# Optimization experiments

Measured on AMD Instinct MI355X. Metric: run time of the kernel, lower is better.

Reference implementation:

```python
import jax, jax.numpy as jnp
import numpy as np

N_Q = 4  # QuantumSampler is hard-wired to 4 qubits (16-dim statevector)


def _build_tables():
    """Static permutation for the CNOT chain and Z-sign table, computed once in numpy."""
    n = N_Q
    dim = 1 << n
    cnots = [(i, (i + 1) % n) for i in range(n)]  # (0,1),(1,2),(2,3),(3,0)
    fmap = np.empty(dim, dtype=np.int64)
    for i in range(dim):
        bits = [(i >> (n - 1 - w)) & 1 for w in range(n)]  # wire w <-> bit (n-1-w)
        for c, t in cnots:
            if bits[c]:
                bits[t] ^= 1
        fmap[i] = sum(b << (n - 1 - w) for w, b in enumerate(bits))
    finv = np.argsort(fmap)  # new_state[j] = old_state[finv[j]]
    signs = np.array([[1.0 - 2.0 * ((j >> (n - 1 - w)) & 1) for w in range(n)]
                      for j in range(dim)], dtype=np.float32)  # <Z_w> signs per basis state
    return jnp.asarray(finv), jnp.asarray(signs)

PERM, SIGNS = _build_tables()


def quantum_gate_probs(q, theta):
    """Simulate: RX(q_w) then RX(theta_w) per wire (angles add), CNOT chain, <Z> per wire, softmax.
    q: [B,4] encoder angles; theta: [4] trainable angles. Returns [B,4] gate probabilities."""
    half = 0.5 * (q + theta)                      # RX(a)RX(b) = RX(a+b)
    c = jnp.cos(half).astype(jnp.complex64)       # amplitude on |0>
    s = (jnp.sin(half).astype(jnp.complex64)) * (-1j)  # amplitude on |1> is -i sin(a/2)
    a = jnp.stack([c, s], axis=-1)                # [B,4,2] single-qubit states
    a0, a1, a2, a3 = a[:, 0], a[:, 1], a[:, 2], a[:, 3]
    # product state |psi> = a0 (x) a1 (x) a2 (x) a3  -> [B,2,2,2,2] -> [B,16]
    st = (a0[:, :, None, None, None] * a1[:, None, :, None, None]
          * a2[:, None, None, :, None] * a3[:, None, None, None, :])
    st = st.reshape(q.shape[0], 16)[:, PERM]      # apply CNOT chain (amplitude permutation)
    probs = st.real ** 2 + st.imag ** 2           # [B,16]
    exps = probs @ SIGNS                          # [B,4] Pauli-Z expectations per wire
    return jax.nn.softmax(exps, axis=-1)


def setup_inputs() -> dict:
    key = jax.random.key(0)
    ks = jax.random.split(key, 8)
    T, B, D, H = 256, 128, 1024, 1024
    inputs = jax.random.normal(ks[0], (T, B, D), dtype=jnp.float32)
    sc_d = 1.0 / np.sqrt(D)
    sc_h = 1.0 / np.sqrt(H)
    return {
        "inputs": inputs,
        "Wi": jax.random.normal(ks[1], (H, D), dtype=jnp.float32) * sc_d,
        "bi": jnp.zeros((H,), dtype=jnp.float32),
        "Wh": jax.random.normal(ks[2], (H, H), dtype=jnp.float32) * sc_h,
        "bh": jnp.zeros((H,), dtype=jnp.float32),
        "Wq": jax.random.normal(ks[3], (4, H), dtype=jnp.float32) * sc_h,
        "bq": jnp.zeros((4,), dtype=jnp.float32),
        "theta": jax.random.uniform(ks[4], (4,), dtype=jnp.float32, minval=-np.pi, maxval=np.pi),
    }


def reference(inputs, Wi, bi, Wh, bh, Wq, bq, theta):
    T, B, _ = inputs.shape
    H = Wi.shape[0]
    hx0 = jnp.zeros((B, H), dtype=inputs.dtype)
    cx0 = jnp.zeros((B, H), dtype=inputs.dtype)

    def step(carry, x):
        hx, cx = carry
        combined = x @ Wi.T + bi + hx @ Wh.T + bh   # [B,H]
        qin = combined @ Wq.T + bq                  # [B,4]
        gates = quantum_gate_probs(qin, theta)      # [B,4]
        f, i_, g, o = gates[:, 0:1], gates[:, 1:2], gates[:, 2:3], gates[:, 3:4]
        cx = f * cx + i_ * jnp.tanh(g)              # broadcast [B,1]*[B,H]
        hx = o * jnp.tanh(cx)
        return (hx, cx), hx

    (hx, cx), ys = jax.lax.scan(step, (hx0, cx0), inputs)
    return ys, hx, cx
```

## Files before the change

kernel.cpp:

```cpp
#include <hip/hip_runtime.h>

#define T_STEPS 256
#define BATCH   128
#define DIM     1024
#define NROWS   (T_STEPS * BATCH)
#define TOTROWS (NROWS + 2 * BATCH)

typedef float vfloat4 __attribute__((ext_vector_type(4)));

#define WS_M     0
#define WS_V     4096
#define WS_CB    4128
#define WS_ZERO_BYTES ((WS_CB + 4) * 4)
#define WS_QX    8192

__global__ __launch_bounds__(256) void k_prep(const float* __restrict__ Wi,
                                              const float* __restrict__ Wh,
                                              const float* __restrict__ bi,
                                              const float* __restrict__ bh,
                                              const float* __restrict__ Wq,
                                              float* __restrict__ M,
                                              float* __restrict__ v,
                                              float* __restrict__ cb) {
    int blk  = blockIdx.x;
    int tid  = threadIdx.x;
    int wave = tid >> 6;
    int lane = tid & 63;

    if (blk < 64) {
        int j0 = blk * 16;
        #pragma unroll
        for (int db = 0; db < 4; db++) {
            int d = db * 256 + tid;
            float a0 = 0.f, a1 = 0.f, a2 = 0.f, a3 = 0.f;
            #pragma unroll 4
            for (int jj = 0; jj < 16; jj++) {
                int j = j0 + jj;
                float wv = Wi[(size_t)j * DIM + d];
                a0 += Wq[0 * DIM + j] * wv;
                a1 += Wq[1 * DIM + j] * wv;
                a2 += Wq[2 * DIM + j] * wv;
                a3 += Wq[3 * DIM + j] * wv;
            }
            unsafeAtomicAdd(&M[0 * DIM + d], a0);
            unsafeAtomicAdd(&M[1 * DIM + d], a1);
            unsafeAtomicAdd(&M[2 * DIM + d], a2);
            unsafeAtomicAdd(&M[3 * DIM + d], a3);
        }
    } else {
        int j0 = (blk - 64) * 16 + wave * 4;
        float sv0 = 0.f, sv1 = 0.f, sv2 = 0.f, sv3 = 0.f;
        float sc0 = 0.f, sc1 = 0.f, sc2 = 0.f, sc3 = 0.f;
        #pragma unroll
        for (int jj = 0; jj < 4; jj++) {
            int j = j0 + jj;
            const float4* row = (const float4*)(Wh + (size_t)j * DIM);
            float s = 0.f;
            #pragma unroll
            for (int k = 0; k < 4; k++) {
                float4 t4 = row[k * 64 + lane];
                s += t4.x + t4.y + t4.z + t4.w;
            }
            #pragma unroll
            for (int off = 32; off; off >>= 1) s += __shfl_xor(s, off, 64);
            float bb = bi[j] + bh[j];
            float q0 = Wq[0 * DIM + j], q1 = Wq[1 * DIM + j];
            float q2 = Wq[2 * DIM + j], q3 = Wq[3 * DIM + j];
            sv0 += q0 * s;  sc0 += q0 * bb;
            sv1 += q1 * s;  sc1 += q1 * bb;
            sv2 += q2 * s;  sc2 += q2 * bb;
            sv3 += q3 * s;  sc3 += q3 * bb;
        }
        if (lane == 0) {
            unsafeAtomicAdd(&v[0], sv0);  unsafeAtomicAdd(&v[1], sv1);
            unsafeAtomicAdd(&v[2], sv2);  unsafeAtomicAdd(&v[3], sv3);
            unsafeAtomicAdd(&cb[0], sc0); unsafeAtomicAdd(&cb[1], sc1);
            unsafeAtomicAdd(&cb[2], sc2); unsafeAtomicAdd(&cb[3], sc3);
        }
    }
}

__global__ __launch_bounds__(256) void k_qx(const float* __restrict__ x,
                                            const float* __restrict__ M,
                                            float4* __restrict__ qx4) {
    int gtid   = blockIdx.x * blockDim.x + threadIdx.x;
    int wave   = gtid >> 6;
    int lane   = threadIdx.x & 63;
    int nwaves = (gridDim.x * blockDim.x) >> 6;

    float4 m[4][4];
    #pragma unroll
    for (int w = 0; w < 4; w++)
        #pragma unroll
        for (int k = 0; k < 4; k++)
            m[w][k] = *(const float4*)(M + w * DIM + k * 256 + lane * 4);

    for (int r = wave; r < NROWS; r += nwaves) {
        const float4* row = (const float4*)(x + (size_t)r * DIM);
        float a0 = 0.f, a1 = 0.f, a2 = 0.f, a3 = 0.f;
        #pragma unroll
        for (int k = 0; k < 4; k++) {
            float4 xv = row[k * 64 + lane];
            a0 += xv.x * m[0][k].x + xv.y * m[0][k].y + xv.z * m[0][k].z + xv.w * m[0][k].w;
            a1 += xv.x * m[1][k].x + xv.y * m[1][k].y + xv.z * m[1][k].z + xv.w * m[1][k].w;
            a2 += xv.x * m[2][k].x + xv.y * m[2][k].y + xv.z * m[2][k].z + xv.w * m[2][k].w;
            a3 += xv.x * m[3][k].x + xv.y * m[3][k].y + xv.z * m[3][k].z + xv.w * m[3][k].w;
        }
        #pragma unroll
        for (int off = 32; off; off >>= 1) {
            a0 += __shfl_xor(a0, off, 64);
            a1 += __shfl_xor(a1, off, 64);
            a2 += __shfl_xor(a2, off, 64);
            a3 += __shfl_xor(a3, off, 64);
        }
        if (lane == 0) qx4[r] = make_float4(a0, a1, a2, a3);
    }
}

__device__ __forceinline__ float fast_tanh(float x) {
    float e = __expf(2.f * x);
    return (e - 1.f) * __builtin_amdgcn_rcpf(e + 1.f);
}

__device__ __forceinline__ void rec_step(float4 q,
                                         float b0, float b1, float b2, float b3,
                                         float v0, float v1, float v2, float v3,
                                         float& h, float& c) {
    float z0 = __cosf(q.x + b0 + h * v0);
    float z1 = __cosf(q.y + b1 + h * v1);
    float z2 = __cosf(q.z + b2 + h * v2);
    float z3 = __cosf(q.w + b3 + h * v3);
    float e1 = z0 * z1;
    float e2 = e1 * z2;
    float e3 = e2 * z3;
    float e0 = z1 * z2 * z3;
    float x0 = __expf(e0), x1 = __expf(e1), x2 = __expf(e2), x3 = __expf(e3);
    float inv = __builtin_amdgcn_rcpf(x0 + x1 + x2 + x3);
    float f  = x0 * inv;
    float i_ = x1 * inv;
    float g  = x2 * inv;
    float o  = x3 * inv;
    c = f * c + i_ * fast_tanh(g);
    h = o * fast_tanh(c);
}

__global__ __launch_bounds__(256) void k_recw(const float* __restrict__ bq,
                                              const float* __restrict__ theta,
                                              const float* __restrict__ v,
                                              const float* __restrict__ cbp,
                                              const float4* __restrict__ qx4,
                                              float* __restrict__ out) {
    const int b    = blockIdx.x;
    const int wave = threadIdx.x >> 6;
    const int lane = threadIdx.x & 63;
    const int foff = wave * 256 + lane * 4;

    float v0 = v[0], v1 = v[1], v2 = v[2], v3 = v[3];
    float b0 = cbp[0] + bq[0] + theta[0];
    float b1 = cbp[1] + bq[1] + theta[1];
    float b2 = cbp[2] + bq[2] + theta[2];
    float b3 = cbp[3] + bq[3] + theta[3];

    float h = 0.f, c = 0.f;

    float4 q0 = qx4[0 * BATCH + b], q1 = qx4[1 * BATCH + b];
    float4 q2 = qx4[2 * BATCH + b], q3 = qx4[3 * BATCH + b];
    float4 q4 = qx4[4 * BATCH + b], q5 = qx4[5 * BATCH + b];
    float4 q6 = qx4[6 * BATCH + b], q7 = qx4[7 * BATCH + b];

    #define EMIT_H(tt)                                                          \
        do {                                                                    \
            vfloat4 vv = {h, h, h, h};                                          \
            __builtin_nontemporal_store(vv,                                     \
                (vfloat4*)(out + ((size_t)(tt) * BATCH + b) * DIM + foff));     \
        } while (0)

    for (int t = 0; t < T_STEPS; t += 8) {
        float4 n0, n1, n2, n3, n4, n5, n6, n7;
        if (t + 8 < T_STEPS) {
            n0 = qx4[(t + 8)  * BATCH + b];  n1 = qx4[(t + 9)  * BATCH + b];
            n2 = qx4[(t + 10) * BATCH + b];  n3 = qx4[(t + 11) * BATCH + b];
            n4 = qx4[(t + 12) * BATCH + b];  n5 = qx4[(t + 13) * BATCH + b];
            n6 = qx4[(t + 14) * BATCH + b];  n7 = qx4[(t + 15) * BATCH + b];
        }
        rec_step(q0, b0, b1, b2, b3, v0, v1, v2, v3, h, c); EMIT_H(t + 0);
        rec_step(q1, b0, b1, b2, b3, v0, v1, v2, v3, h, c); EMIT_H(t + 1);
        rec_step(q2, b0, b1, b2, b3, v0, v1, v2, v3, h, c); EMIT_H(t + 2);
        rec_step(q3, b0, b1, b2, b3, v0, v1, v2, v3, h, c); EMIT_H(t + 3);
        rec_step(q4, b0, b1, b2, b3, v0, v1, v2, v3, h, c); EMIT_H(t + 4);
        rec_step(q5, b0, b1, b2, b3, v0, v1, v2, v3, h, c); EMIT_H(t + 5);
        rec_step(q6, b0, b1, b2, b3, v0, v1, v2, v3, h, c); EMIT_H(t + 6);
        rec_step(q7, b0, b1, b2, b3, v0, v1, v2, v3, h, c); EMIT_H(t + 7);
        q0 = n0; q1 = n1; q2 = n2; q3 = n3; q4 = n4; q5 = n5; q6 = n6; q7 = n7;
    }
    #undef EMIT_H

    vfloat4 hv = {h, h, h, h};
    vfloat4 cv = {c, c, c, c};
    __builtin_nontemporal_store(hv,
        (vfloat4*)(out + ((size_t)NROWS + b) * DIM + foff));
    __builtin_nontemporal_store(cv,
        (vfloat4*)(out + ((size_t)NROWS + BATCH + b) * DIM + foff));
}

extern "C" void kernel_launch(void* const* d_in, const int* in_sizes, int n_in,
                              void* d_out, int out_size, void* d_ws, size_t ws_size,
                              hipStream_t stream) {
    const float* inputs = (const float*)d_in[0];
    const float* Wi     = (const float*)d_in[1];
    const float* bi     = (const float*)d_in[2];
    const float* Wh     = (const float*)d_in[3];
    const float* bh     = (const float*)d_in[4];
    const float* Wq     = (const float*)d_in[5];
    const float* bq     = (const float*)d_in[6];
    const float* theta  = (const float*)d_in[7];
    float* out = (float*)d_out;
    float* ws  = (float*)d_ws;

    float*  M    = ws + WS_M;
    float*  v    = ws + WS_V;
    float*  cb   = ws + WS_CB;
    float4* qx4  = (float4*)(ws + WS_QX);

    (void)hipMemsetAsync(ws, 0, WS_ZERO_BYTES, stream);
    k_prep <<<128,   256, 0, stream>>>(Wi, Wh, bi, bh, Wq, M, v, cb);
    k_qx   <<<1024,  256, 0, stream>>>(inputs, M, qx4);
    k_recw <<<BATCH, 256, 0, stream>>>(bq, theta, v, cb, qx4, out);
}
```

Baseline: 303.2 us.

## Fuse prep, projection and recurrence into one persistent kernel with flag sync

Merges the three kernels into a single 1024-block launch. Prep blocks signal a global counter, projection waves compute qx rows in iteration groups and signal per-group counters, and 128 recurrence blocks spin-wait on those counters so the recurrence overlaps the streaming projection. This removes launch gaps and the serialisation between projection and recurrence. It relies on all blocks being co-resident, since spin-waits could deadlock otherwise, and it adds atomic and polling overhead.

```diff
diff --git a/kernel.cpp b/kernel.cpp
--- a/kernel.cpp
+++ b/kernel.cpp
@@ -4,116 +4,46 @@
 #define BATCH   128
 #define DIM     1024
 #define NROWS   (T_STEPS * BATCH)
-#define TOTROWS (NROWS + 2 * BATCH)
+
+#define NBLK    1024
+#define NTHR    256
+
+#define PREP_BLKS 128
+#define REC_BLK0  128
+#define QX_BLK0   256
+#define QX_BLOCKS 896
+#define QX_WAVES  3584
+#define NITER     10
 
 typedef float vfloat4 __attribute__((ext_vector_type(4)));
 
 #define WS_M     0
 #define WS_V     4096
 #define WS_CB    4128
-#define WS_ZERO_BYTES ((WS_CB + 4) * 4)
+#define WS_C1    4136
+#define WS_CNT   4140
+#define WS_ZERO_BYTES (4152 * 4)
 #define WS_QX    8192
 
-__global__ __launch_bounds__(256) void k_prep(const float* __restrict__ Wi,
-                                              const float* __restrict__ Wh,
-                                              const float* __restrict__ bi,
-                                              const float* __restrict__ bh,
-                                              const float* __restrict__ Wq,
-                                              float* __restrict__ M,
-                                              float* __restrict__ v,
-                                              float* __restrict__ cb) {
-    int blk  = blockIdx.x;
-    int tid  = threadIdx.x;
-    int wave = tid >> 6;
-    int lane = tid & 63;
-
-    if (blk < 64) {
-        int j0 = blk * 16;
-        #pragma unroll
-        for (int db = 0; db < 4; db++) {
-            int d = db * 256 + tid;
-            float a0 = 0.f, a1 = 0.f, a2 = 0.f, a3 = 0.f;
-            #pragma unroll 4
-            for (int jj = 0; jj < 16; jj++) {
-                int j = j0 + jj;
-                float wv = Wi[(size_t)j * DIM + d];
-                a0 += Wq[0 * DIM + j] * wv;
-                a1 += Wq[1 * DIM + j] * wv;
-                a2 += Wq[2 * DIM + j] * wv;
-                a3 += Wq[3 * DIM + j] * wv;
-            }
-            unsafeAtomicAdd(&M[0 * DIM + d], a0);
-            unsafeAtomicAdd(&M[1 * DIM + d], a1);
-            unsafeAtomicAdd(&M[2 * DIM + d], a2);
-            unsafeAtomicAdd(&M[3 * DIM + d], a3);
-        }
-    } else {
-        int j0 = (blk - 64) * 16 + wave * 4;
-        float sv0 = 0.f, sv1 = 0.f, sv2 = 0.f, sv3 = 0.f;
-        float sc0 = 0.f, sc1 = 0.f, sc2 = 0.f, sc3 = 0.f;
-        #pragma unroll
-        for (int jj = 0; jj < 4; jj++) {
-            int j = j0 + jj;
-            const float4* row = (const float4*)(Wh + (size_t)j * DIM);
-            float s = 0.f;
-            #pragma unroll
-            for (int k = 0; k < 4; k++) {
-                float4 t4 = row[k * 64 + lane];
-                s += t4.x + t4.y + t4.z + t4.w;
-            }
-            #pragma unroll
-            for (int off = 32; off; off >>= 1) s += __shfl_xor(s, off, 64);
-            float bb = bi[j] + bh[j];
-            float q0 = Wq[0 * DIM + j], q1 = Wq[1 * DIM + j];
-            float q2 = Wq[2 * DIM + j], q3 = Wq[3 * DIM + j];
-            sv0 += q0 * s;  sc0 += q0 * bb;
-            sv1 += q1 * s;  sc1 += q1 * bb;
-            sv2 += q2 * s;  sc2 += q2 * bb;
-            sv3 += q3 * s;  sc3 += q3 * bb;
-        }
-        if (lane == 0) {
-            unsafeAtomicAdd(&v[0], sv0);  unsafeAtomicAdd(&v[1], sv1);
-            unsafeAtomicAdd(&v[2], sv2);  unsafeAtomicAdd(&v[3], sv3);
-            unsafeAtomicAdd(&cb[0], sc0); unsafeAtomicAdd(&cb[1], sc1);
-            unsafeAtomicAdd(&cb[2], sc2); unsafeAtomicAdd(&cb[3], sc3);
-        }
-    }
-}
-
-__global__ __launch_bounds__(256) void k_qx(const float* __restrict__ x,
-                                            const float* __restrict__ M,
-                                            float4* __restrict__ qx4) {
-    int gtid   = blockIdx.x * blockDim.x + threadIdx.x;
-    int wave   = gtid >> 6;
-    int lane   = threadIdx.x & 63;
-    int nwaves = (gridDim.x * blockDim.x) >> 6;
-
-    float4 m[4][4];
-    #pragma unroll
-    for (int w = 0; w < 4; w++)
-        #pragma unroll
-        for (int k = 0; k < 4; k++)
-            m[w][k] = *(const float4*)(M + w * DIM + k * 256 + lane * 4);
-
-    for (int r = wave; r < NROWS; r += nwaves) {
-        const float4* row = (const float4*)(x + (size_t)r * DIM);
-        float a0 = 0.f, a1 = 0.f, a2 = 0.f, a3 = 0.f;
-        #pragma unroll
-        for (int k = 0; k < 4; k++) {
-            float4 xv = row[k * 64 + lane];
-            a0 += xv.x * m[0][k].x + xv.y * m[0][k].y + xv.z * m[0][k].z + xv.w * m[0][k].w;
-            a1 += xv.x * m[1][k].x + xv.y * m[1][k].y + xv.z * m[1][k].z + xv.w * m[1][k].w;
-            a2 += xv.x * m[2][k].x + xv.y * m[2][k].y + xv.z * m[2][k].z + xv.w * m[2][k].w;
-            a3 += xv.x * m[3][k].x + xv.y * m[3][k].y + xv.z * m[3][k].z + xv.w * m[3][k].w;
-        }
-        #pragma unroll
-        for (int off = 32; off; off >>= 1) {
-            a0 += __shfl_xor(a0, off, 64);
-            a1 += __shfl_xor(a1, off, 64);
-            a2 += __shfl_xor(a2, off, 64);
-            a3 += __shfl_xor(a3, off, 64);
-        }
-        if (lane == 0) qx4[r] = make_float4(a0, a1, a2, a3);
+__device__ __forceinline__ void spin_geq(const unsigned* p, unsigned target) {
+    for (int k = 0; k < (1 << 22); ++k) {
+        if (__hip_atomic_load(p, __ATOMIC_ACQUIRE, __HIP_MEMORY_SCOPE_AGENT) >= target)
+            return;
+        __builtin_amdgcn_s_sleep(2);
+    }
+}
+
+__device__ __forceinline__ void block_wait(const unsigned* p, unsigned target) {
+    if (threadIdx.x == 0) spin_geq(p, target);
+    __syncthreads();
+    __threadfence();
+}
+
+__device__ __forceinline__ void block_signal(unsigned* p) {
+    __syncthreads();
+    if (threadIdx.x == 0) {
+        __threadfence();
+        atomicAdd(p, 1u);
     }
 }
 
@@ -144,63 +74,184 @@
     h = o * fast_tanh(c);
 }
 
-__global__ __launch_bounds__(256) void k_recw(const float* __restrict__ bq,
-                                              const float* __restrict__ theta,
-                                              const float* __restrict__ v,
-                                              const float* __restrict__ cbp,
-                                              const float4* __restrict__ qx4,
-                                              float* __restrict__ out) {
-    const int b    = blockIdx.x;
-    const int wave = threadIdx.x >> 6;
-    const int lane = threadIdx.x & 63;
-    const int foff = wave * 256 + lane * 4;
-
-    float v0 = v[0], v1 = v[1], v2 = v[2], v3 = v[3];
-    float b0 = cbp[0] + bq[0] + theta[0];
-    float b1 = cbp[1] + bq[1] + theta[1];
-    float b2 = cbp[2] + bq[2] + theta[2];
-    float b3 = cbp[3] + bq[3] + theta[3];
-
-    float h = 0.f, c = 0.f;
-
-    float4 q0 = qx4[0 * BATCH + b], q1 = qx4[1 * BATCH + b];
-    float4 q2 = qx4[2 * BATCH + b], q3 = qx4[3 * BATCH + b];
-    float4 q4 = qx4[4 * BATCH + b], q5 = qx4[5 * BATCH + b];
-    float4 q6 = qx4[6 * BATCH + b], q7 = qx4[7 * BATCH + b];
-
-    #define EMIT_H(tt)                                                          \
-        do {                                                                    \
-            vfloat4 vv = {h, h, h, h};                                          \
-            __builtin_nontemporal_store(vv,                                     \
-                (vfloat4*)(out + ((size_t)(tt) * BATCH + b) * DIM + foff));     \
-        } while (0)
-
-    for (int t = 0; t < T_STEPS; t += 8) {
-        float4 n0, n1, n2, n3, n4, n5, n6, n7;
-        if (t + 8 < T_STEPS) {
-            n0 = qx4[(t + 8)  * BATCH + b];  n1 = qx4[(t + 9)  * BATCH + b];
-            n2 = qx4[(t + 10) * BATCH + b];  n3 = qx4[(t + 11) * BATCH + b];
-            n4 = qx4[(t + 12) * BATCH + b];  n5 = qx4[(t + 13) * BATCH + b];
-            n6 = qx4[(t + 14) * BATCH + b];  n7 = qx4[(t + 15) * BATCH + b];
-        }
-        rec_step(q0, b0, b1, b2, b3, v0, v1, v2, v3, h, c); EMIT_H(t + 0);
-        rec_step(q1, b0, b1, b2, b3, v0, v1, v2, v3, h, c); EMIT_H(t + 1);
-        rec_step(q2, b0, b1, b2, b3, v0, v1, v2, v3, h, c); EMIT_H(t + 2);
-        rec_step(q3, b0, b1, b2, b3, v0, v1, v2, v3, h, c); EMIT_H(t + 3);
-        rec_step(q4, b0, b1, b2, b3, v0, v1, v2, v3, h, c); EMIT_H(t + 4);
-        rec_step(q5, b0, b1, b2, b3, v0, v1, v2, v3, h, c); EMIT_H(t + 5);
-        rec_step(q6, b0, b1, b2, b3, v0, v1, v2, v3, h, c); EMIT_H(t + 6);
-        rec_step(q7, b0, b1, b2, b3, v0, v1, v2, v3, h, c); EMIT_H(t + 7);
-        q0 = n0; q1 = n1; q2 = n2; q3 = n3; q4 = n4; q5 = n5; q6 = n6; q7 = n7;
-    }
-    #undef EMIT_H
-
-    vfloat4 hv = {h, h, h, h};
-    vfloat4 cv = {c, c, c, c};
-    __builtin_nontemporal_store(hv,
-        (vfloat4*)(out + ((size_t)NROWS + b) * DIM + foff));
-    __builtin_nontemporal_store(cv,
-        (vfloat4*)(out + ((size_t)NROWS + BATCH + b) * DIM + foff));
+__global__ __launch_bounds__(NTHR) void k_fused(
+        const float* __restrict__ x,
+        const float* __restrict__ Wi,
+        const float* __restrict__ bi,
+        const float* __restrict__ Wh,
+        const float* __restrict__ bh,
+        const float* __restrict__ Wq,
+        const float* __restrict__ bq,
+        const float* __restrict__ theta,
+        float* __restrict__ ws,
+        float* __restrict__ out)
+{
+    float*    M    = ws + WS_M;
+    float*    v    = ws + WS_V;
+    float*    cb   = ws + WS_CB;
+    unsigned* c1   = (unsigned*)(ws + WS_C1);
+    unsigned* cnt  = (unsigned*)(ws + WS_CNT);
+    float4*   qx4  = (float4*)(ws + WS_QX);
+
+    const int blk  = blockIdx.x;
+    const int tid  = threadIdx.x;
+    const int wave = tid >> 6;
+    const int lane = tid & 63;
+
+    if (blk < 64) {
+        int j0 = blk * 16;
+        #pragma unroll
+        for (int db = 0; db < 4; db++) {
+            int d = db * 256 + tid;
+            float a0 = 0.f, a1 = 0.f, a2 = 0.f, a3 = 0.f;
+            #pragma unroll 4
+            for (int jj = 0; jj < 16; jj++) {
+                int j = j0 + jj;
+                float wv = Wi[(size_t)j * DIM + d];
+                a0 += Wq[0 * DIM + j] * wv;
+                a1 += Wq[1 * DIM + j] * wv;
+                a2 += Wq[2 * DIM + j] * wv;
+                a3 += Wq[3 * DIM + j] * wv;
+            }
+            unsafeAtomicAdd(&M[0 * DIM + d], a0);
+            unsafeAtomicAdd(&M[1 * DIM + d], a1);
+            unsafeAtomicAdd(&M[2 * DIM + d], a2);
+            unsafeAtomicAdd(&M[3 * DIM + d], a3);
+        }
+        block_signal(c1);
+    } else if (blk < PREP_BLKS) {
+        int j0 = (blk - 64) * 16 + wave * 4;
+        float sv0 = 0.f, sv1 = 0.f, sv2 = 0.f, sv3 = 0.f;
+        float sc0 = 0.f, sc1 = 0.f, sc2 = 0.f, sc3 = 0.f;
+        #pragma unroll
+        for (int jj = 0; jj < 4; jj++) {
+            int j = j0 + jj;
+            const float4* row = (const float4*)(Wh + (size_t)j * DIM);
+            float s = 0.f;
+            #pragma unroll
+            for (int k = 0; k < 4; k++) {
+                float4 t4 = row[k * 64 + lane];
+                s += t4.x + t4.y + t4.z + t4.w;
+            }
+            #pragma unroll
+            for (int off = 32; off; off >>= 1) s += __shfl_xor(s, off, 64);
+            float bb = bi[j] + bh[j];
+            float q0 = Wq[0 * DIM + j], q1 = Wq[1 * DIM + j];
+            float q2 = Wq[2 * DIM + j], q3 = Wq[3 * DIM + j];
+            sv0 += q0 * s;  sc0 += q0 * bb;
+            sv1 += q1 * s;  sc1 += q1 * bb;
+            sv2 += q2 * s;  sc2 += q2 * bb;
+            sv3 += q3 * s;  sc3 += q3 * bb;
+        }
+        if (lane == 0) {
+            unsafeAtomicAdd(&v[0], sv0);  unsafeAtomicAdd(&v[1], sv1);
+            unsafeAtomicAdd(&v[2], sv2);  unsafeAtomicAdd(&v[3], sv3);
+            unsafeAtomicAdd(&cb[0], sc0); unsafeAtomicAdd(&cb[1], sc1);
+            unsafeAtomicAdd(&cb[2], sc2); unsafeAtomicAdd(&cb[3], sc3);
+        }
+        block_signal(c1);
+    }
+
+    if (blk >= REC_BLK0 && blk < REC_BLK0 + BATCH) {
+        block_wait(c1, PREP_BLKS);
+        const int b    = blk - REC_BLK0;
+        const int foff = wave * 256 + lane * 4;
+
+        float v0 = v[0], v1 = v[1], v2 = v[2], v3 = v[3];
+        float b0 = cb[0] + bq[0] + theta[0];
+        float b1 = cb[1] + bq[1] + theta[1];
+        float b2 = cb[2] + bq[2] + theta[2];
+        float b3 = cb[3] + bq[3] + theta[3];
+
+        float h = 0.f, c = 0.f;
+        float4 q0, q1, q2, q3, q4, q5, q6, q7;
+
+        #define EMIT_H(tt)                                                          \
+            do {                                                                    \
+                vfloat4 vv = {h, h, h, h};                                          \
+                __builtin_nontemporal_store(vv,                                     \
+                    (vfloat4*)(out + ((size_t)(tt) * BATCH + b) * DIM + foff));     \
+            } while (0)
+
+        for (int gt = 0; gt < T_STEPS / 32; ++gt) {
+            int r_hi = (gt * 32 + 40) * BATCH;
+            if (r_hi > NROWS) r_hi = NROWS;
+            int g = (r_hi + QX_WAVES - 1) / QX_WAVES - 1;
+            if (g >= NITER) g = NITER - 1;
+            block_wait(&cnt[g], QX_BLOCKS);
+
+            if (gt == 0) {
+                q0 = qx4[0 * BATCH + b]; q1 = qx4[1 * BATCH + b];
+                q2 = qx4[2 * BATCH + b]; q3 = qx4[3 * BATCH + b];
+                q4 = qx4[4 * BATCH + b]; q5 = qx4[5 * BATCH + b];
+                q6 = qx4[6 * BATCH + b]; q7 = qx4[7 * BATCH + b];
+            }
+            for (int t = gt * 32; t < gt * 32 + 32; t += 8) {
+                float4 n0, n1, n2, n3, n4, n5, n6, n7;
+                if (t + 8 < T_STEPS) {
+                    n0 = qx4[(t + 8)  * BATCH + b];  n1 = qx4[(t + 9)  * BATCH + b];
+                    n2 = qx4[(t + 10) * BATCH + b];  n3 = qx4[(t + 11) * BATCH + b];
+                    n4 = qx4[(t + 12) * BATCH + b];  n5 = qx4[(t + 13) * BATCH + b];
+                    n6 = qx4[(t + 14) * BATCH + b];  n7 = qx4[(t + 15) * BATCH + b];
+                }
+                rec_step(q0, b0, b1, b2, b3, v0, v1, v2, v3, h, c); EMIT_H(t + 0);
+                rec_step(q1, b0, b1, b2, b3, v0, v1, v2, v3, h, c); EMIT_H(t + 1);
+                rec_step(q2, b0, b1, b2, b3, v0, v1, v2, v3, h, c); EMIT_H(t + 2);
+                rec_step(q3, b0, b1, b2, b3, v0, v1, v2, v3, h, c); EMIT_H(t + 3);
+                rec_step(q4, b0, b1, b2, b3, v0, v1, v2, v3, h, c); EMIT_H(t + 4);
+                rec_step(q5, b0, b1, b2, b3, v0, v1, v2, v3, h, c); EMIT_H(t + 5);
+                rec_step(q6, b0, b1, b2, b3, v0, v1, v2, v3, h, c); EMIT_H(t + 6);
+                rec_step(q7, b0, b1, b2, b3, v0, v1, v2, v3, h, c); EMIT_H(t + 7);
+                q0 = n0; q1 = n1; q2 = n2; q3 = n3; q4 = n4; q5 = n5; q6 = n6; q7 = n7;
+            }
+        }
+        #undef EMIT_H
+
+        vfloat4 hv = {h, h, h, h};
+        vfloat4 cv = {c, c, c, c};
+        __builtin_nontemporal_store(hv,
+            (vfloat4*)(out + ((size_t)NROWS + b) * DIM + foff));
+        __builtin_nontemporal_store(cv,
+            (vfloat4*)(out + ((size_t)NROWS + BATCH + b) * DIM + foff));
+        return;
+    }
+
+    block_wait(c1, PREP_BLKS);
+
+    const int qxw = (blk < PREP_BLKS) ? (blk * 4 + wave)
+                                      : (512 + (blk - QX_BLK0) * 4 + wave);
+
+    float4 m[4][4];
+    #pragma unroll
+    for (int w = 0; w < 4; w++)
+        #pragma unroll
+        for (int k = 0; k < 4; k++)
+            m[w][k] = *(const float4*)(M + w * DIM + k * 256 + lane * 4);
+
+    for (int g = 0; g < NITER; ++g) {
+        int r = qxw + g * QX_WAVES;
+        if (r < NROWS) {
+            const float4* row = (const float4*)(x + (size_t)r * DIM);
+            float a0 = 0.f, a1 = 0.f, a2 = 0.f, a3 = 0.f;
+            #pragma unroll
+            for (int k = 0; k < 4; k++) {
+                float4 xv = row[k * 64 + lane];
+                a0 += xv.x * m[0][k].x + xv.y * m[0][k].y + xv.z * m[0][k].z + xv.w * m[0][k].w;
+                a1 += xv.x * m[1][k].x + xv.y * m[1][k].y + xv.z * m[1][k].z + xv.w * m[1][k].w;
+                a2 += xv.x * m[2][k].x + xv.y * m[2][k].y + xv.z * m[2][k].z + xv.w * m[2][k].w;
+                a3 += xv.x * m[3][k].x + xv.y * m[3][k].y + xv.z * m[3][k].z + xv.w * m[3][k].w;
+            }
+            #pragma unroll
+            for (int off = 32; off; off >>= 1) {
+                a0 += __shfl_xor(a0, off, 64);
+                a1 += __shfl_xor(a1, off, 64);
+                a2 += __shfl_xor(a2, off, 64);
+                a3 += __shfl_xor(a3, off, 64);
+            }
+            if (lane == 0) qx4[r] = make_float4(a0, a1, a2, a3);
+        }
+        block_signal(&cnt[g]);
+    }
 }
 
 extern "C" void kernel_launch(void* const* d_in, const int* in_sizes, int n_in,
@@ -217,13 +268,7 @@
     float* out = (float*)d_out;
     float* ws  = (float*)d_ws;
 
-    float*  M    = ws + WS_M;
-    float*  v    = ws + WS_V;
-    float*  cb   = ws + WS_CB;
-    float4* qx4  = (float4*)(ws + WS_QX);
-
     (void)hipMemsetAsync(ws, 0, WS_ZERO_BYTES, stream);
-    k_prep <<<128,   256, 0, stream>>>(Wi, Wh, bi, bh, Wq, M, v, cb);
-    k_qx   <<<1024,  256, 0, stream>>>(inputs, M, qx4);
-    k_recw <<<BATCH, 256, 0, stream>>>(bq, theta, v, cb, qx4, out);
-}
+
+    k_fused<<<NBLK, NTHR, 0, stream>>>(inputs, Wi, bi, Wh, bh, Wq, bq, theta, ws, out);
+}
```

New measurement: 1.023 ms. 237% more time.

## Fuse qx projection and recurrence into one kernel with counter-based producer/consumer sync

Applied to the files above, without the earlier changes.

Merges the input-projection kernel and the recurrent kernel into a single launch. 128 blocks run the recurrence while the remaining blocks compute qx rows and bump per-iteration completion counters, which the recurrence blocks poll before prefetching the next timesteps. The aim is to overlap the recurrence and its large output writes with the streaming input projection. The cost is spin-wait polling, a dependence on all blocks being co-resident, and relaxed atomics with no explicit release/acquire fences, so memory ordering is fragile.

```diff
diff --git a/kernel.cpp b/kernel.cpp
--- a/kernel.cpp
+++ b/kernel.cpp
@@ -4,14 +4,21 @@
 #define BATCH   128
 #define DIM     1024
 #define NROWS   (T_STEPS * BATCH)
-#define TOTROWS (NROWS + 2 * BATCH)
+
+#define NBLK    1024
+#define NTHR    256
+#define REC_BLKS 128
+#define QX_BLKS  (NBLK - REC_BLKS)
+#define QX_WAVES (QX_BLKS * 4)
+#define NITER    ((NROWS + QX_WAVES - 1) / QX_WAVES)
 
 typedef float vfloat4 __attribute__((ext_vector_type(4)));
 
 #define WS_M     0
 #define WS_V     4096
 #define WS_CB    4128
-#define WS_ZERO_BYTES ((WS_CB + 4) * 4)
+#define WS_CNT   4136
+#define WS_ZERO_BYTES ((WS_CNT + NITER) * 4)
 #define WS_QX    8192
 
 __global__ __launch_bounds__(256) void k_prep(const float* __restrict__ Wi,
@@ -80,43 +87,6 @@
     }
 }
 
-__global__ __launch_bounds__(256) void k_qx(const float* __restrict__ x,
-                                            const float* __restrict__ M,
-                                            float4* __restrict__ qx4) {
-    int gtid   = blockIdx.x * blockDim.x + threadIdx.x;
-    int wave   = gtid >> 6;
-    int lane   = threadIdx.x & 63;
-    int nwaves = (gridDim.x * blockDim.x) >> 6;
-
-    float4 m[4][4];
-    #pragma unroll
-    for (int w = 0; w < 4; w++)
-        #pragma unroll
-        for (int k = 0; k < 4; k++)
-            m[w][k] = *(const float4*)(M + w * DIM + k * 256 + lane * 4);
-
-    for (int r = wave; r < NROWS; r += nwaves) {
-        const float4* row = (const float4*)(x + (size_t)r * DIM);
-        float a0 = 0.f, a1 = 0.f, a2 = 0.f, a3 = 0.f;
-        #pragma unroll
-        for (int k = 0; k < 4; k++) {
-            float4 xv = row[k * 64 + lane];
-            a0 += xv.x * m[0][k].x + xv.y * m[0][k].y + xv.z * m[0][k].z + xv.w * m[0][k].w;
-            a1 += xv.x * m[1][k].x + xv.y * m[1][k].y + xv.z * m[1][k].z + xv.w * m[1][k].w;
-            a2 += xv.x * m[2][k].x + xv.y * m[2][k].y + xv.z * m[2][k].z + xv.w * m[2][k].w;
-            a3 += xv.x * m[3][k].x + xv.y * m[3][k].y + xv.z * m[3][k].z + xv.w * m[3][k].w;
-        }
-        #pragma unroll
-        for (int off = 32; off; off >>= 1) {
-            a0 += __shfl_xor(a0, off, 64);
-            a1 += __shfl_xor(a1, off, 64);
-            a2 += __shfl_xor(a2, off, 64);
-            a3 += __shfl_xor(a3, off, 64);
-        }
-        if (lane == 0) qx4[r] = make_float4(a0, a1, a2, a3);
-    }
-}
-
 __device__ __forceinline__ float fast_tanh(float x) {
     float e = __expf(2.f * x);
     return (e - 1.f) * __builtin_amdgcn_rcpf(e + 1.f);
@@ -144,16 +114,83 @@
     h = o * fast_tanh(c);
 }
 
-__global__ __launch_bounds__(256) void k_recw(const float* __restrict__ bq,
-                                              const float* __restrict__ theta,
-                                              const float* __restrict__ v,
-                                              const float* __restrict__ cbp,
-                                              const float4* __restrict__ qx4,
-                                              float* __restrict__ out) {
-    const int b    = blockIdx.x;
-    const int wave = threadIdx.x >> 6;
-    const int lane = threadIdx.x & 63;
-    const int foff = wave * 256 + lane * 4;
+__device__ __forceinline__ void wait_cnt(const unsigned* p, unsigned target) {
+    if (threadIdx.x == 0) {
+        for (int k = 0; k < (1 << 20); ++k) {
+            if (__hip_atomic_load(p, __ATOMIC_RELAXED, __HIP_MEMORY_SCOPE_AGENT) >= target)
+                break;
+            __builtin_amdgcn_s_sleep(8);
+        }
+    }
+    __syncthreads();
+    asm volatile("" ::: "memory");
+}
+
+__global__ __launch_bounds__(NTHR) void k_main(const float* __restrict__ x,
+                                               const float* __restrict__ bq,
+                                               const float* __restrict__ theta,
+                                               const float* __restrict__ v,
+                                               const float* __restrict__ cbp,
+                                               float* __restrict__ ws,
+                                               float* __restrict__ out)
+{
+    float*    M   = ws + WS_M;
+    unsigned* cnt = (unsigned*)(ws + WS_CNT);
+    float4*   qx4 = (float4*)(ws + WS_QX);
+
+    const int blk  = blockIdx.x;
+    const int tid  = threadIdx.x;
+    const int wave = tid >> 6;
+    const int lane = tid & 63;
+
+    if (blk >= REC_BLKS) {
+        const int w = (blk - REC_BLKS) * 4 + wave;
+
+        float4 m[4][4];
+        #pragma unroll
+        for (int ww = 0; ww < 4; ww++)
+            #pragma unroll
+            for (int k = 0; k < 4; k++)
+                m[ww][k] = *(const float4*)(M + ww * DIM + k * 256 + lane * 4);
+
+        for (int g = 0; g < NITER; ++g) {
+            int r = w + g * QX_WAVES;
+            if (r < NROWS) {
+                const float4* row = (const float4*)(x + (size_t)r * DIM);
+                float a0 = 0.f, a1 = 0.f, a2 = 0.f, a3 = 0.f;
+                #pragma unroll
+                for (int k = 0; k < 4; k++) {
+                    float4 xv = row[k * 64 + lane];
+                    a0 += xv.x * m[0][k].x + xv.y * m[0][k].y + xv.z * m[0][k].z + xv.w * m[0][k].w;
+                    a1 += xv.x * m[1][k].x + xv.y * m[1][k].y + xv.z * m[1][k].z + xv.w * m[1][k].w;
+                    a2 += xv.x * m[2][k].x + xv.y * m[2][k].y + xv.z * m[2][k].z + xv.w * m[2][k].w;
+                    a3 += xv.x * m[3][k].x + xv.y * m[3][k].y + xv.z * m[3][k].z + xv.w * m[3][k].w;
+                }
+                #pragma unroll
+                for (int off = 32; off; off >>= 1) {
+                    a0 += __shfl_xor(a0, off, 64);
+                    a1 += __shfl_xor(a1, off, 64);
+                    a2 += __shfl_xor(a2, off, 64);
+                    a3 += __shfl_xor(a3, off, 64);
+                }
+                if (lane == 0) {
+                    unsigned long long lo = (unsigned long long)__float_as_uint(a0)
+                                          | ((unsigned long long)__float_as_uint(a1) << 32);
+                    unsigned long long hi = (unsigned long long)__float_as_uint(a2)
+                                          | ((unsigned long long)__float_as_uint(a3) << 32);
+                    unsigned long long* p = (unsigned long long*)&qx4[r];
+                    __hip_atomic_store(p,     lo, __ATOMIC_RELAXED, __HIP_MEMORY_SCOPE_AGENT);
+                    __hip_atomic_store(p + 1, hi, __ATOMIC_RELAXED, __HIP_MEMORY_SCOPE_AGENT);
+                }
+            }
+            __syncthreads();
+            if (tid == 0)
+                __hip_atomic_fetch_add(&cnt[g], 1u, __ATOMIC_RELAXED, __HIP_MEMORY_SCOPE_AGENT);
+        }
+        return;
+    }
+
+    const int b = blk;
 
     float v0 = v[0], v1 = v[1], v2 = v[2], v3 = v[3];
     float b0 = cbp[0] + bq[0] + theta[0];
@@ -163,21 +200,26 @@
 
     float h = 0.f, c = 0.f;
 
+    #define EMIT_H(tt)                                                      \
+        do {                                                                \
+            vfloat4 vv = {h, h, h, h};                                      \
+            __builtin_nontemporal_store(vv,                                 \
+                (vfloat4*)(out + ((size_t)(tt) * BATCH + b) * DIM) + tid);  \
+        } while (0)
+
+    wait_cnt(&cnt[0], QX_BLKS);
+
     float4 q0 = qx4[0 * BATCH + b], q1 = qx4[1 * BATCH + b];
     float4 q2 = qx4[2 * BATCH + b], q3 = qx4[3 * BATCH + b];
     float4 q4 = qx4[4 * BATCH + b], q5 = qx4[5 * BATCH + b];
     float4 q6 = qx4[6 * BATCH + b], q7 = qx4[7 * BATCH + b];
 
-    #define EMIT_H(tt)                                                          \
-        do {                                                                    \
-            vfloat4 vv = {h, h, h, h};                                          \
-            __builtin_nontemporal_store(vv,                                     \
-                (vfloat4*)(out + ((size_t)(tt) * BATCH + b) * DIM + foff));     \
-        } while (0)
-
     for (int t = 0; t < T_STEPS; t += 8) {
         float4 n0, n1, n2, n3, n4, n5, n6, n7;
         if (t + 8 < T_STEPS) {
+            int last_row = (t + 16) * BATCH - 1;
+            if (last_row >= NROWS) last_row = NROWS - 1;
+            wait_cnt(&cnt[last_row / QX_WAVES], QX_BLKS);
             n0 = qx4[(t + 8)  * BATCH + b];  n1 = qx4[(t + 9)  * BATCH + b];
             n2 = qx4[(t + 10) * BATCH + b];  n3 = qx4[(t + 11) * BATCH + b];
             n4 = qx4[(t + 12) * BATCH + b];  n5 = qx4[(t + 13) * BATCH + b];
@@ -197,10 +239,8 @@
 
     vfloat4 hv = {h, h, h, h};
     vfloat4 cv = {c, c, c, c};
-    __builtin_nontemporal_store(hv,
-        (vfloat4*)(out + ((size_t)NROWS + b) * DIM + foff));
-    __builtin_nontemporal_store(cv,
-        (vfloat4*)(out + ((size_t)NROWS + BATCH + b) * DIM + foff));
+    __builtin_nontemporal_store(hv, (vfloat4*)(out + ((size_t)NROWS + b) * DIM) + tid);
+    __builtin_nontemporal_store(cv, (vfloat4*)(out + ((size_t)NROWS + BATCH + b) * DIM) + tid);
 }
 
 extern "C" void kernel_launch(void* const* d_in, const int* in_sizes, int n_in,
@@ -217,13 +257,12 @@
     float* out = (float*)d_out;
     float* ws  = (float*)d_ws;
 
-    float*  M    = ws + WS_M;
-    float*  v    = ws + WS_V;
-    float*  cb   = ws + WS_CB;
-    float4* qx4  = (float4*)(ws + WS_QX);
+    float* M  = ws + WS_M;
+    float* v  = ws + WS_V;
+    float* cb = ws + WS_CB;
 
     (void)hipMemsetAsync(ws, 0, WS_ZERO_BYTES, stream);
-    k_prep <<<128,   256, 0, stream>>>(Wi, Wh, bi, bh, Wq, M, v, cb);
-    k_qx   <<<1024,  256, 0, stream>>>(inputs, M, qx4);
-    k_recw <<<BATCH, 256, 0, stream>>>(bq, theta, v, cb, qx4, out);
-}
+
+    k_prep<<<128,  256, 0, stream>>>(Wi, Wh, bi, bh, Wq, M, v, cb);
+    k_main<<<NBLK, 256, 0, stream>>>(inputs, bq, theta, v, cb, ws, out);
+}
```

After: 460.5 us. +51.9%, slower.

## Replace atomics and memset with deterministic partial sums; split recurrence across more blocks

Applied to the files above, without the earlier changes.

The prep kernel now computes M directly per column with no atomics, and writes per-block partial sums of v and cb that the recurrence kernel reduces itself. This removes the memset launch and the atomic traffic. The recurrence kernel now launches 512 single-wave blocks, each handling a quarter of the output row for one batch element, so more CUs take part in writing the large output. The cost is that every block redundantly recomputes the scalar recurrence and the partial-sum reduction, and the M computation is now a long serial loop over only 16 blocks.

```diff
diff --git a/kernel.cpp b/kernel.cpp
--- a/kernel.cpp
+++ b/kernel.cpp
@@ -4,14 +4,11 @@
 #define BATCH   128
 #define DIM     1024
 #define NROWS   (T_STEPS * BATCH)
-#define TOTROWS (NROWS + 2 * BATCH)
 
 typedef float vfloat4 __attribute__((ext_vector_type(4)));
 
 #define WS_M     0
-#define WS_V     4096
-#define WS_CB    4128
-#define WS_ZERO_BYTES ((WS_CB + 4) * 4)
+#define WS_VP    4096
 #define WS_QX    8192
 
 __global__ __launch_bounds__(256) void k_prep(const float* __restrict__ Wi,
@@ -20,35 +17,26 @@
                                               const float* __restrict__ bh,
                                               const float* __restrict__ Wq,
                                               float* __restrict__ M,
-                                              float* __restrict__ v,
-                                              float* __restrict__ cb) {
+                                              float* __restrict__ vpart) {
     int blk  = blockIdx.x;
     int tid  = threadIdx.x;
     int wave = tid >> 6;
     int lane = tid & 63;
 
-    if (blk < 64) {
-        int j0 = blk * 16;
-        #pragma unroll
-        for (int db = 0; db < 4; db++) {
-            int d = db * 256 + tid;
-            float a0 = 0.f, a1 = 0.f, a2 = 0.f, a3 = 0.f;
-            #pragma unroll 4
-            for (int jj = 0; jj < 16; jj++) {
-                int j = j0 + jj;
-                float wv = Wi[(size_t)j * DIM + d];
-                a0 += Wq[0 * DIM + j] * wv;
-                a1 += Wq[1 * DIM + j] * wv;
-                a2 += Wq[2 * DIM + j] * wv;
-                a3 += Wq[3 * DIM + j] * wv;
-            }
-            unsafeAtomicAdd(&M[0 * DIM + d], a0);
-            unsafeAtomicAdd(&M[1 * DIM + d], a1);
-            unsafeAtomicAdd(&M[2 * DIM + d], a2);
-            unsafeAtomicAdd(&M[3 * DIM + d], a3);
-        }
+    if (blk < 16) {
+        int d = blk * 64 + lane;
+        const float* wq = Wq + wave * DIM;
+        float acc = 0.f;
+        for (int j = 0; j < DIM; j += 8) {
+            #pragma unroll
+            for (int u = 0; u < 8; u++)
+                acc += wq[j + u] * Wi[(size_t)(j + u) * DIM + d];
+        }
+        M[wave * DIM + d] = acc;
     } else {
-        int j0 = (blk - 64) * 16 + wave * 4;
+        int bb = blk - 16;
+        __shared__ float red[4][8];
+        int j0 = bb * 16 + wave * 4;
         float sv0 = 0.f, sv1 = 0.f, sv2 = 0.f, sv3 = 0.f;
         float sc0 = 0.f, sc1 = 0.f, sc2 = 0.f, sc3 = 0.f;
         #pragma unroll
@@ -63,20 +51,21 @@
             }
             #pragma unroll
             for (int off = 32; off; off >>= 1) s += __shfl_xor(s, off, 64);
-            float bb = bi[j] + bh[j];
+            float bbias = bi[j] + bh[j];
             float q0 = Wq[0 * DIM + j], q1 = Wq[1 * DIM + j];
             float q2 = Wq[2 * DIM + j], q3 = Wq[3 * DIM + j];
-            sv0 += q0 * s;  sc0 += q0 * bb;
-            sv1 += q1 * s;  sc1 += q1 * bb;
-            sv2 += q2 * s;  sc2 += q2 * bb;
-            sv3 += q3 * s;  sc3 += q3 * bb;
+            sv0 += q0 * s;  sc0 += q0 * bbias;
+            sv1 += q1 * s;  sc1 += q1 * bbias;
+            sv2 += q2 * s;  sc2 += q2 * bbias;
+            sv3 += q3 * s;  sc3 += q3 * bbias;
         }
         if (lane == 0) {
-            unsafeAtomicAdd(&v[0], sv0);  unsafeAtomicAdd(&v[1], sv1);
-            unsafeAtomicAdd(&v[2], sv2);  unsafeAtomicAdd(&v[3], sv3);
-            unsafeAtomicAdd(&cb[0], sc0); unsafeAtomicAdd(&cb[1], sc1);
-            unsafeAtomicAdd(&cb[2], sc2); unsafeAtomicAdd(&cb[3], sc3);
-        }
+            red[wave][0] = sv0; red[wave][1] = sv1; red[wave][2] = sv2; red[wave][3] = sv3;
+            red[wave][4] = sc0; red[wave][5] = sc1; red[wave][6] = sc2; red[wave][7] = sc3;
+        }
+        __syncthreads();
+        if (tid < 8)
+            vpart[bb * 8 + tid] = red[0][tid] + red[1][tid] + red[2][tid] + red[3][tid];
     }
 }
 
@@ -122,14 +111,14 @@
     return (e - 1.f) * __builtin_amdgcn_rcpf(e + 1.f);
 }
 
-__device__ __forceinline__ void rec_step(float4 q,
+__device__ __forceinline__ void rec_step(float4 qv,
                                          float b0, float b1, float b2, float b3,
                                          float v0, float v1, float v2, float v3,
                                          float& h, float& c) {
-    float z0 = __cosf(q.x + b0 + h * v0);
-    float z1 = __cosf(q.y + b1 + h * v1);
-    float z2 = __cosf(q.z + b2 + h * v2);
-    float z3 = __cosf(q.w + b3 + h * v3);
+    float z0 = __cosf(qv.x + b0 + h * v0);
+    float z1 = __cosf(qv.y + b1 + h * v1);
+    float z2 = __cosf(qv.z + b2 + h * v2);
+    float z3 = __cosf(qv.w + b3 + h * v3);
     float e1 = z0 * z1;
     float e2 = e1 * z2;
     float e3 = e2 * z3;
@@ -144,36 +133,46 @@
     h = o * fast_tanh(c);
 }
 
-__global__ __launch_bounds__(256) void k_recw(const float* __restrict__ bq,
-                                              const float* __restrict__ theta,
-                                              const float* __restrict__ v,
-                                              const float* __restrict__ cbp,
-                                              const float4* __restrict__ qx4,
-                                              float* __restrict__ out) {
-    const int b    = blockIdx.x;
-    const int wave = threadIdx.x >> 6;
-    const int lane = threadIdx.x & 63;
-    const int foff = wave * 256 + lane * 4;
-
-    float v0 = v[0], v1 = v[1], v2 = v[2], v3 = v[3];
-    float b0 = cbp[0] + bq[0] + theta[0];
-    float b1 = cbp[1] + bq[1] + theta[1];
-    float b2 = cbp[2] + bq[2] + theta[2];
-    float b3 = cbp[3] + bq[3] + theta[3];
+__global__ __launch_bounds__(64) void k_recw(const float* __restrict__ bq,
+                                             const float* __restrict__ theta,
+                                             const float* __restrict__ ws,
+                                             float* __restrict__ out) {
+    const float4* qx4 = (const float4*)(ws + WS_QX);
+    const float4* vp4 = (const float4*)(ws + WS_VP);
+
+    const int b    = blockIdx.x & 127;
+    const int q    = blockIdx.x >> 7;
+    const int lane = threadIdx.x;
+
+    float4 sa = vp4[lane * 2];
+    float4 sc = vp4[lane * 2 + 1];
+    #pragma unroll
+    for (int off = 32; off; off >>= 1) {
+        sa.x += __shfl_xor(sa.x, off, 64);  sa.y += __shfl_xor(sa.y, off, 64);
+        sa.z += __shfl_xor(sa.z, off, 64);  sa.w += __shfl_xor(sa.w, off, 64);
+        sc.x += __shfl_xor(sc.x, off, 64);  sc.y += __shfl_xor(sc.y, off, 64);
+        sc.z += __shfl_xor(sc.z, off, 64);  sc.w += __shfl_xor(sc.w, off, 64);
+    }
+    const float v0 = sa.x, v1 = sa.y, v2 = sa.z, v3 = sa.w;
+    const float b0 = sc.x + bq[0] + theta[0];
+    const float b1 = sc.y + bq[1] + theta[1];
+    const float b2 = sc.z + bq[2] + theta[2];
+    const float b3 = sc.w + bq[3] + theta[3];
 
     float h = 0.f, c = 0.f;
+
+    #define EMIT_H(tt)                                                           \
+        do {                                                                     \
+            vfloat4 vv = {h, h, h, h};                                           \
+            __builtin_nontemporal_store(vv,                                      \
+                (vfloat4*)(out + ((size_t)(tt) * BATCH + b) * DIM + q * 256)     \
+                    + lane);                                                     \
+        } while (0)
 
     float4 q0 = qx4[0 * BATCH + b], q1 = qx4[1 * BATCH + b];
     float4 q2 = qx4[2 * BATCH + b], q3 = qx4[3 * BATCH + b];
     float4 q4 = qx4[4 * BATCH + b], q5 = qx4[5 * BATCH + b];
     float4 q6 = qx4[6 * BATCH + b], q7 = qx4[7 * BATCH + b];
-
-    #define EMIT_H(tt)                                                          \
-        do {                                                                    \
-            vfloat4 vv = {h, h, h, h};                                          \
-            __builtin_nontemporal_store(vv,                                     \
-                (vfloat4*)(out + ((size_t)(tt) * BATCH + b) * DIM + foff));     \
-        } while (0)
 
     for (int t = 0; t < T_STEPS; t += 8) {
         float4 n0, n1, n2, n3, n4, n5, n6, n7;
@@ -198,9 +197,9 @@
     vfloat4 hv = {h, h, h, h};
     vfloat4 cv = {c, c, c, c};
     __builtin_nontemporal_store(hv,
-        (vfloat4*)(out + ((size_t)NROWS + b) * DIM + foff));
+        (vfloat4*)(out + ((size_t)NROWS + b) * DIM + q * 256) + lane);
     __builtin_nontemporal_store(cv,
-        (vfloat4*)(out + ((size_t)NROWS + BATCH + b) * DIM + foff));
+        (vfloat4*)(out + ((size_t)NROWS + BATCH + b) * DIM + q * 256) + lane);
 }
 
 extern "C" void kernel_launch(void* const* d_in, const int* in_sizes, int n_in,
@@ -217,13 +216,11 @@
     float* out = (float*)d_out;
     float* ws  = (float*)d_ws;
 
-    float*  M    = ws + WS_M;
-    float*  v    = ws + WS_V;
-    float*  cb   = ws + WS_CB;
-    float4* qx4  = (float4*)(ws + WS_QX);
-
-    (void)hipMemsetAsync(ws, 0, WS_ZERO_BYTES, stream);
-    k_prep <<<128,   256, 0, stream>>>(Wi, Wh, bi, bh, Wq, M, v, cb);
-    k_qx   <<<1024,  256, 0, stream>>>(inputs, M, qx4);
-    k_recw <<<BATCH, 256, 0, stream>>>(bq, theta, v, cb, qx4, out);
-}
+    float*  M     = ws + WS_M;
+    float*  vpart = ws + WS_VP;
+    float4* qx4   = (float4*)(ws + WS_QX);
+
+    k_prep<<<80,   256, 0, stream>>>(Wi, Wh, bi, bh, Wq, M, vpart);
+    k_qx  <<<1024, 256, 0, stream>>>(inputs, M, qx4);
+    k_recw<<<512,  64,  0, stream>>>(bq, theta, ws, out);
+}
```

Measured after the change: 318.4 us. +5.0%, slower.
